# Kernel tuning notes

Hardware: AMD Instinct MI355X
Metric: run time of the kernel (lower is better)

The kernel has to match this reference:

```python
import jax, jax.numpy as jnp
import numpy as np

HIDDEN = 2048
N_HEADS = 32
N_KV = 8
HEAD_DIM = 64
ROPE_THETA = 10000.0


def setup_inputs() -> dict:
    key = jax.random.key(0)
    k0, k1, k2, k3, k4 = jax.random.split(key, 5)
    B, S = 2, 2048
    scale_in = 1.0 / np.sqrt(HIDDEN)
    return {
        "hidden_states": jax.random.normal(k0, (B, S, HIDDEN), dtype=jnp.float32),
        # weights stored [in, out] (transpose of torch Linear.weight)
        "Wq": jax.random.normal(k1, (HIDDEN, N_HEADS * HEAD_DIM), dtype=jnp.float32) * scale_in,
        "Wk": jax.random.normal(k2, (HIDDEN, N_KV * HEAD_DIM), dtype=jnp.float32) * scale_in,
        "Wv": jax.random.normal(k3, (HIDDEN, N_KV * HEAD_DIM), dtype=jnp.float32) * scale_in,
        "Wo": jax.random.normal(k4, (N_HEADS * HEAD_DIM, HIDDEN), dtype=jnp.float32) * scale_in,
    }


def _rope_tables(seq_len, dim, theta):
    inv_freq = 1.0 / (theta ** (jnp.arange(0, dim, 2, dtype=jnp.float32) / dim))
    t = jnp.arange(seq_len, dtype=jnp.float32)
    freqs = jnp.outer(t, inv_freq)              # [S, D/2]
    emb = jnp.concatenate([freqs, freqs], -1)   # [S, D]
    return jnp.cos(emb), jnp.sin(emb)


def _rotate_half(x):
    d = x.shape[-1] // 2
    return jnp.concatenate([-x[..., d:], x[..., :d]], axis=-1)


def reference(hidden_states, Wq, Wk, Wv, Wo):
    B, S, _ = hidden_states.shape
    G = N_HEADS // N_KV  # groups per kv head

    q = (hidden_states @ Wq).reshape(B, S, N_HEADS, HEAD_DIM).transpose(0, 2, 1, 3)  # [B,H,S,D]
    k = (hidden_states @ Wk).reshape(B, S, N_KV, HEAD_DIM).transpose(0, 2, 1, 3)     # [B,KV,S,D]
    v = (hidden_states @ Wv).reshape(B, S, N_KV, HEAD_DIM).transpose(0, 2, 1, 3)

    cos, sin = _rope_tables(S, HEAD_DIM, ROPE_THETA)  # [S,D]
    q = q * cos + _rotate_half(q) * sin
    k = k * cos + _rotate_half(k) * sin

    # GQA without materializing repeated KV: fold q heads into [KV, G]
    qg = q.reshape(B, N_KV, G, S, HEAD_DIM)
    scale = HEAD_DIM ** -0.5
    scores = jnp.einsum("bkgsd,bktd->bkgst", qg, k) * scale  # [B,KV,G,S,S]

    causal = jnp.tril(jnp.ones((S, S), dtype=bool))
    scores = jnp.where(causal, scores, jnp.float32(-1e30))
    probs = jax.nn.softmax(scores, axis=-1)

    out = jnp.einsum("bkgst,bktd->bkgsd", probs, v)          # [B,KV,G,S,D]
    out = out.reshape(B, N_HEADS, S, HEAD_DIM).transpose(0, 2, 1, 3).reshape(B, S, N_HEADS * HEAD_DIM)
    return out @ Wo
```

## Files before the change

kernel.cpp:

```cpp
#include <hip/hip_runtime.h>
#include <cstdint>
#include <cstddef>

typedef __attribute__((ext_vector_type(8))) short short8;
typedef __attribute__((ext_vector_type(4))) float f32x4;
typedef __attribute__((ext_vector_type(16))) float f32x16;

#define MFMA16(a, b, c) __builtin_amdgcn_mfma_f32_16x16x32_bf16((a), (b), (c), 0, 0, 0)
#define MFMA32(a, b, c) __builtin_amdgcn_mfma_f32_32x32x16_bf16((a), (b), (c), 0, 0, 0)

union F2U { float f; unsigned int u; };
union U4S8 { uint4 u4; unsigned short s[8]; short8 v; };

__device__ __forceinline__ unsigned short f2bf(float f) {
  F2U x; x.f = f;
  unsigned int r = x.u + 0x7fffu + ((x.u >> 16) & 1u);
  return (unsigned short)(r >> 16);
}
__device__ __forceinline__ float bf2f(unsigned short s) {
  F2U x; x.u = ((unsigned int)s) << 16;
  return x.f;
}
__device__ __forceinline__ float fexp2(float x) {
  float r; asm("v_exp_f32 %0, %1" : "=v"(r) : "v"(x)); return r;
}
__device__ __forceinline__ unsigned int cvtpk(float lo, float hiv) {
  unsigned int r; asm("v_cvt_pk_bf16_f32 %0, %1, %2" : "=v"(r) : "v"(lo), "v"(hiv)); return r;
}

#define HIDDEN 2048
#define NHEADS 32
#define NKV 8
#define HDIM 64
#define SEQ 2048
#define BATCH 2
#define NTOK (BATCH * SEQ)
#define QKVN 3072
#define QSCALE 0.18033688011117309f

__global__ __launch_bounds__(256) void prep_kernel(const float* __restrict__ X,
                                                   const float* __restrict__ Wq,
                                                   const float* __restrict__ Wk,
                                                   const float* __restrict__ Wv,
                                                   const float* __restrict__ Wo,
                                                   unsigned short* __restrict__ Xb,
                                                   unsigned short* __restrict__ Wqkv_t,
                                                   unsigned short* __restrict__ Wot,
                                                   float* __restrict__ ct,
                                                   float* __restrict__ st) {
  __shared__ unsigned short lt[64][72];
  int bid = blockIdx.x;
  const int t = threadIdx.x;

  if (bid < 256) {
    int idx = bid * 256 + t;
    int s = idx >> 5;
    int i = idx & 31;
    float invf = expf(-(float)i * (9.210340371976184f / 32.0f));
    float f = (float)s * invf;
    ct[idx] = cosf(f);
    st[idx] = sinf(f);
    return;
  }
  bid -= 256;
  if (bid < 4096) {
    size_t i = ((size_t)bid * 256 + t) * 8;
    float4 a0 = *(const float4*)(X + i);
    float4 a1 = *(const float4*)(X + i + 4);
    U4S8 p;
    p.s[0] = f2bf(a0.x); p.s[1] = f2bf(a0.y); p.s[2] = f2bf(a0.z); p.s[3] = f2bf(a0.w);
    p.s[4] = f2bf(a1.x); p.s[5] = f2bf(a1.y); p.s[6] = f2bf(a1.z); p.s[7] = f2bf(a1.w);
    *(short8*)(Xb + i) = p.v;
    return;
  }
  bid -= 4096;
  const float* W; unsigned short* Wt; int N, row_off, bx, by;
  if (bid < 1024)      { W = Wq; Wt = Wqkv_t; N = 2048; row_off = 0;    bx = bid & 31; by = bid >> 5; }
  else if (bid < 1280) { bid -= 1024; W = Wk; Wt = Wqkv_t; N = 512; row_off = 2048; bx = bid & 7; by = bid >> 3; }
  else if (bid < 1536) { bid -= 1280; W = Wv; Wt = Wqkv_t; N = 512; row_off = 2560; bx = bid & 7; by = bid >> 3; }
  else                 { bid -= 1536; W = Wo; Wt = Wot;    N = 2048; row_off = 0;   bx = bid & 31; by = bid >> 5; }
  const int k0 = by * 64, n0 = bx * 64;
  #pragma unroll
  for (int p = 0; p < 4; ++p) {
    int kr = p * 16 + (t >> 4);
    int nc = (t & 15) * 4;
    float4 v = *(const float4*)&W[(size_t)(k0 + kr) * N + n0 + nc];
    lt[nc + 0][kr] = f2bf(v.x);
    lt[nc + 1][kr] = f2bf(v.y);
    lt[nc + 2][kr] = f2bf(v.z);
    lt[nc + 3][kr] = f2bf(v.w);
  }
  __syncthreads();
  #pragma unroll
  for (int p = 0; p < 2; ++p) {
    int nr = p * 32 + (t >> 3);
    int kc = (t & 7) * 8;
    *(short8*)&Wt[(size_t)(row_off + n0 + nr) * HIDDEN + k0 + kc] = *(const short8*)&lt[nr][kc];
  }
}

template<int MODE>
__global__ __launch_bounds__(256) void gemm128_kernel(const unsigned short* __restrict__ Ab,
                                                      const unsigned short* __restrict__ Bt,
                                                      void* __restrict__ Cp,
                                                      int M, int N, int K,
                                                      const float* __restrict__ ct,
                                                      const float* __restrict__ st) {
  __shared__ __align__(16) unsigned short lds_a[128][64];
  __shared__ __align__(16) unsigned short lds_b[128][64];

  const int t = threadIdx.x, lane = t & 63, w = t >> 6;
  const int q32 = lane & 31, hi = lane >> 5;

  const int orig = blockIdx.y * gridDim.x + blockIdx.x;
  const int nwg  = (int)(gridDim.x * gridDim.y);
  const int cpx  = nwg >> 3;
  const int swz  = (orig & 7) * cpx + (orig >> 3);
  const int m0 = (swz / (int)gridDim.x) * 128;
  const int n0 = (swz % (int)gridDim.x) * 128;

  const int wr = (w >> 1) * 64, wc = (w & 1) * 64;

  f32x16 acc[2][2] = {};

  for (int k0 = 0; k0 < K; k0 += 64) {
    __syncthreads();
    #pragma unroll
    for (int c = 0; c < 4; ++c) {
      int row = w * 32 + c * 8 + (lane >> 3);
      int cks = (lane & 7) ^ (row & 7);
      __builtin_amdgcn_global_load_lds(
          (const __attribute__((address_space(1))) unsigned int*)(Ab + (size_t)(m0 + row) * K + k0 + cks * 8),
          (__attribute__((address_space(3))) unsigned int*)&lds_a[w * 32 + c * 8][0], 16, 0, 0);
      __builtin_amdgcn_global_load_lds(
          (const __attribute__((address_space(1))) unsigned int*)(Bt + (size_t)(n0 + row) * K + k0 + cks * 8),
          (__attribute__((address_space(3))) unsigned int*)&lds_b[w * 32 + c * 8][0], 16, 0, 0);
    }
    __syncthreads();

    #pragma unroll
    for (int kq = 0; kq < 4; ++kq) {
      short8 af[2], bf[2];
      #pragma unroll
      for (int i = 0; i < 2; ++i) {
        int row = wr + i * 32 + q32;
        af[i] = *(const short8*)((const char*)&lds_a[0][0] + row * 128 + (((kq * 2 + hi) ^ (row & 7)) * 16));
      }
      #pragma unroll
      for (int j = 0; j < 2; ++j) {
        int row = wc + j * 32 + q32;
        bf[j] = *(const short8*)((const char*)&lds_b[0][0] + row * 128 + (((kq * 2 + hi) ^ (row & 7)) * 16));
      }
      acc[0][0] = MFMA32(af[0], bf[0], acc[0][0]);
      acc[0][1] = MFMA32(af[0], bf[1], acc[0][1]);
      acc[1][0] = MFMA32(af[1], bf[0], acc[1][0]);
      acc[1][1] = MFMA32(af[1], bf[1], acc[1][1]);
    }
  }

  if constexpr (MODE == 0) {
    #pragma unroll
    for (int i = 0; i < 2; ++i)
      #pragma unroll
      for (int j = 0; j < 2; ++j)
        #pragma unroll
        for (int r = 0; r < 16; ++r) {
          int row = m0 + wr + i * 32 + (r & 3) + 8 * (r >> 2) + 4 * hi;
          int col = n0 + wc + j * 32 + q32;
          ((float*)Cp)[(size_t)row * N + col] = acc[i][j][r];
        }
  } else {
    const bool isV = (n0 >= 2560);
    const bool isQ = (n0 < 2048);
    #pragma unroll
    for (int i = 0; i < 2; ++i)
      #pragma unroll
      for (int r = 0; r < 16; ++r) {
        int row = m0 + wr + i * 32 + (r & 3) + 8 * (r >> 2) + 4 * hi;
        int s_tok = row & (SEQ - 1);
        float cc = 0.f, ss = 0.f;
        if (!isV) {
          cc = ct[s_tok * 32 + q32];
          ss = st[s_tok * 32 + q32];
        }
        #pragma unroll
        for (int j = 0; j < 2; ++j) {
          int col = n0 + wc + j * 32 + q32;
          float v = acc[i][j][r];
          float o;
          if (isV) {
            o = v;
          } else {
            float pp = acc[i][j ^ 1][r];
            o = (j == 0) ? (v * cc - pp * ss) : (v * cc + pp * ss);
            if (isQ) o *= QSCALE;
          }
          ((unsigned short*)Cp)[(size_t)row * N + col] = f2bf(o);
        }
      }
  }
}

__global__ __launch_bounds__(256) void v_pack_kernel(const unsigned short* __restrict__ QKV,
                                                     unsigned short* __restrict__ Vt) {
  int idx = blockIdx.x * 256 + threadIdx.x;
  int m = idx >> 9;
  int c = idx & 511;
  int b = m >> 11, s = m & 2047;
  int kv = c >> 6, d = c & 63;
  Vt[(((size_t)(b * NKV + kv)) * HDIM + d) * SEQ + s] = QKV[(size_t)m * QKVN + 2560 + c];
}

#define KVBLK 64

__global__ __launch_bounds__(512, 4) void flash_kernel(const unsigned short* __restrict__ QKV,
                                                       const unsigned short* __restrict__ Vt,
                                                       unsigned short* __restrict__ Ob) {
  const int bx = blockIdx.x;
  const int h = blockIdx.y;
  const int b = blockIdx.z;
  const int kv = h >> 2;
  const int t = threadIdx.x;
  const int lane = t & 63;
  const int w = t >> 6;
  const int p = w >> 1;
  const int kh = w & 1;
  const int q = lane & 31;
  const int hi = lane >> 5;

  __shared__ __align__(16) char smem[34816];
  unsigned short* Klds = (unsigned short*)smem;
  unsigned short* Vlds = (unsigned short*)(smem + 16384);
  float* mlArea = (float*)(smem + 32768);

  const unsigned short* Kg = QKV + (size_t)b * SEQ * QKVN + 2048 + kv * 64;
  const unsigned short* Vg = Vt + ((size_t)(b * NKV + kv)) * HDIM * SEQ;
  const unsigned short* Qh = QKV + (size_t)b * SEQ * QKVN + h * 64;

  const int srow = w * 8 + (lane >> 3);
  const int scks = (lane & 7) ^ (srow & 7);
  const unsigned short* Ksrc = Kg + (size_t)srow * QKVN + scks * 8;
  const unsigned short* Vsrc = Vg + (size_t)srow * SEQ + scks * 8;

  #define STAGE_KV(buf, kt0)                                                              \
    do {                                                                                  \
      __builtin_amdgcn_global_load_lds(                                                   \
          (const __attribute__((address_space(1))) unsigned int*)(Ksrc + (size_t)(kt0) * QKVN), \
          (__attribute__((address_space(3))) unsigned int*)(Klds + (buf) * 4096 + w * 512), 16, 0, 0); \
      __builtin_amdgcn_global_load_lds(                                                   \
          (const __attribute__((address_space(1))) unsigned int*)(Vsrc + (kt0)),          \
          (__attribute__((address_space(3))) unsigned int*)(Vlds + (buf) * 4096 + w * 512), 16, 0, 0); \
    } while (0)

  #pragma unroll 1
  for (int seg = 0; seg < 2; ++seg) {
    const int qb = seg ? bx : (15 - bx);
    const int wq0 = qb * 128 + p * 32;

    short8 qf[4];
    #pragma unroll
    for (int f = 0; f < 4; ++f)
      qf[f] = *(const short8*)&Qh[(size_t)(wq0 + q) * QKVN + f * 16 + hi * 8];

    f32x16 o0 = {}, o1 = {};
    float m_run = -1e30f, l_run = 0.f;

    const int nt_blk = qb * 2 + 2;

    __syncthreads();
    STAGE_KV(0, 0);
    __syncthreads();
    int cur = 0;

    for (int tt = 0; tt < nt_blk; ++tt) {
      if (tt + 1 < nt_blk) STAGE_KV(cur ^ 1, (tt + 1) * KVBLK);

      const int kbase = tt * KVBLK + kh * 32;
      if (kbase <= wq0 + 31) {
        const unsigned short* Kt = Klds + cur * 4096;
        const unsigned short* Vl = Vlds + cur * 4096;

        f32x16 s = {};
        __builtin_amdgcn_s_setprio(1);
        #pragma unroll
        for (int f = 0; f < 4; ++f) {
          short8 kf = *(const short8*)(Kt + (kh * 32 + q) * 64 + (((f * 2 + hi) ^ (q & 7)) * 8));
          s = MFMA32(kf, qf[f], s);
        }
        __builtin_amdgcn_s_setprio(0);

        if (kbase + 31 > wq0) {
          #pragma unroll
          for (int r = 0; r < 16; ++r) {
            int kl = (r & 3) + 8 * (r >> 2) + 4 * hi;
            if (kbase + kl > wq0 + q) s[r] = -1e30f;
          }
        }

        float mt = -1e30f;
        #pragma unroll
        for (int r = 0; r < 16; ++r) mt = fmaxf(mt, s[r]);
        mt = fmaxf(mt, __shfl_xor(mt, 32, 64));

        const bool resc = __any(mt > m_run + 11.0f);
        if (resc) {
          float mn = fmaxf(m_run, mt);
          float alpha = fexp2(m_run - mn);
          m_run = mn;
          l_run *= alpha;
          #pragma unroll
          for (int r = 0; r < 16; ++r) { o0[r] *= alpha; o1[r] *= alpha; }
        }
        float ls = 0.f;
        #pragma unroll
        for (int r = 0; r < 16; ++r) {
          float pp = fexp2(s[r] - m_run);
          s[r] = pp;
          ls += pp;
        }
        ls += __shfl_xor(ls, 32, 64);
        l_run += ls;

        unsigned int own[8];
        #pragma unroll
        for (int g = 0; g < 8; ++g)
          own[g] = cvtpk(s[2 * g], s[2 * g + 1]);

        __builtin_amdgcn_s_setprio(1);
        {
          unsigned int pa0 = own[0], pb0 = own[2];
          unsigned int pa1 = own[1], pb1 = own[3];
          asm("v_permlane32_swap_b32 %0, %1" : "+v"(pa0), "+v"(pb0));
          asm("v_permlane32_swap_b32 %0, %1" : "+v"(pa1), "+v"(pb1));
          U4S8 pfv;
          pfv.u4.x = pa0;
          pfv.u4.y = pa1;
          pfv.u4.z = pb0;
          pfv.u4.w = pb1;
          int co = ((kh * 4 + hi) ^ (q & 7)) * 8;
          short8 vf0 = *(const short8*)(Vl + q * 64 + co);
          short8 vf1 = *(const short8*)(Vl + (32 + q) * 64 + co);
          o0 = MFMA32(vf0, pfv.v, o0);
          o1 = MFMA32(vf1, pfv.v, o1);
        }
        {
          unsigned int pa0 = own[4], pb0 = own[6];
          unsigned int pa1 = own[5], pb1 = own[7];
          asm("v_permlane32_swap_b32 %0, %1" : "+v"(pa0), "+v"(pb0));
          asm("v_permlane32_swap_b32 %0, %1" : "+v"(pa1), "+v"(pb1));
          U4S8 pfv;
          pfv.u4.x = pa0;
          pfv.u4.y = pa1;
          pfv.u4.z = pb0;
          pfv.u4.w = pb1;
          int co = ((kh * 4 + 2 + hi) ^ (q & 7)) * 8;
          short8 vf0 = *(const short8*)(Vl + q * 64 + co);
          short8 vf1 = *(const short8*)(Vl + (32 + q) * 64 + co);
          o0 = MFMA32(vf0, pfv.v, o0);
          o1 = MFMA32(vf1, pfv.v, o1);
        }
        __builtin_amdgcn_s_setprio(0);
      }

      __syncthreads();
      cur ^= 1;
    }

    if (hi == 0) {
      mlArea[(w * 32 + q) * 2 + 0] = m_run;
      mlArea[(w * 32 + q) * 2 + 1] = l_run;
    }
    __syncthreads();
    const int wo = p * 2 + (kh ^ 1);
    float m_oth = mlArea[(wo * 32 + q) * 2 + 0];
    float l_oth = mlArea[(wo * 32 + q) * 2 + 1];
    float m_tot = fmaxf(m_run, m_oth);
    float alf = fexp2(m_run - m_tot);
    float l_tot = l_run * alf + l_oth * fexp2(m_oth - m_tot);
    #pragma unroll
    for (int r = 0; r < 16; ++r) { o0[r] *= alf; o1[r] *= alf; }

    float* oArea = (float*)smem + (size_t)p * 2048;
    if (kh == 1) {
      float* dst = oArea + lane * 32;
      #pragma unroll
      for (int r = 0; r < 16; ++r) { dst[r] = o0[r]; dst[16 + r] = o1[r]; }
    }
    __syncthreads();
    if (kh == 0) {
      const float* src = oArea + lane * 32;
      #pragma unroll
      for (int r = 0; r < 16; ++r) { o0[r] += src[r]; o1[r] += src[16 + r]; }
    }
    __syncthreads();

    if (kh == 0) {
      unsigned short* lo = (unsigned short*)smem + (size_t)p * 2304;
      float inv = 1.0f / l_tot;
      #pragma unroll
      for (int gg = 0; gg < 8; ++gg) {
        int r = 2 * gg;
        int dl = (r & 3) + 8 * (r >> 2) + 4 * hi;
        unsigned int w0 = (unsigned int)f2bf(o0[r] * inv) | ((unsigned int)f2bf(o0[r + 1] * inv) << 16);
        unsigned int w1 = (unsigned int)f2bf(o1[r] * inv) | ((unsigned int)f2bf(o1[r + 1] * inv) << 16);
        *(unsigned int*)&lo[q * 72 + dl] = w0;
        *(unsigned int*)&lo[q * 72 + 32 + dl] = w1;
      }
      {
        int row = lane >> 1;
        int ch = (lane & 1) * 32;
        uint4 x0 = *(const uint4*)&lo[row * 72 + ch + 0];
        uint4 x1 = *(const uint4*)&lo[row * 72 + ch + 8];
        uint4 x2 = *(const uint4*)&lo[row * 72 + ch + 16];
        uint4 x3 = *(const uint4*)&lo[row * 72 + ch + 24];
        unsigned short* dst = &Ob[(size_t)(b * SEQ + wq0 + row) * (NHEADS * HDIM) + h * HDIM + ch];
        *(uint4*)(dst + 0)  = x0;
        *(uint4*)(dst + 8)  = x1;
        *(uint4*)(dst + 16) = x2;
        *(uint4*)(dst + 24) = x3;
      }
    }
  }
}

extern "C" void kernel_launch(void* const* d_in, const int* in_sizes, int n_in,
                              void* d_out, int out_size, void* d_ws, size_t ws_size,
                              hipStream_t stream) {
  const float* X  = (const float*)d_in[0];
  const float* Wq = (const float*)d_in[1];
  const float* Wk = (const float*)d_in[2];
  const float* Wv = (const float*)d_in[3];
  const float* Wo = (const float*)d_in[4];
  float* out = (float*)d_out;

  char* ws = (char*)d_ws;
  size_t off = 0;
  auto carve = [&](size_t bytes) -> void* {
    void* p = ws + off;
    off += (bytes + 255) & ~(size_t)255;
    return p;
  };
  float* rope_cos = (float*)carve((size_t)SEQ * 32 * 4);
  float* rope_sin = (float*)carve((size_t)SEQ * 32 * 4);
  unsigned short* Xb     = (unsigned short*)carve((size_t)NTOK * HIDDEN * 2);
  unsigned short* Wqkv_t = (unsigned short*)carve((size_t)QKVN * HIDDEN * 2);
  unsigned short* Wot    = (unsigned short*)carve((size_t)HIDDEN * HIDDEN * 2);
  unsigned short* QKVb   = (unsigned short*)carve((size_t)NTOK * QKVN * 2);
  unsigned short* Vt     = (unsigned short*)carve((size_t)BATCH * NKV * HDIM * SEQ * 2);
  unsigned short* Ob     = Xb;

  prep_kernel<<<dim3(6912), dim3(256), 0, stream>>>(
      X, Wq, Wk, Wv, Wo, Xb, Wqkv_t, Wot, rope_cos, rope_sin);

  gemm128_kernel<1><<<dim3(QKVN / 128, NTOK / 128), dim3(256), 0, stream>>>(
      Xb, Wqkv_t, QKVb, NTOK, QKVN, HIDDEN, rope_cos, rope_sin);

  v_pack_kernel<<<dim3((NTOK * NKV * HDIM) / 256), dim3(256), 0, stream>>>(QKVb, Vt);

  flash_kernel<<<dim3(8, NHEADS, BATCH), dim3(512), 0, stream>>>(QKVb, Vt, Ob);

  gemm128_kernel<0><<<dim3(HIDDEN / 128, NTOK / 128), dim3(256), 0, stream>>>(
      Ob, Wot, out, NTOK, HIDDEN, HIDDEN, nullptr, nullptr);
}
```

Before: 203.5 us.

## Use 256x256 double-buffered direct-to-LDS GEMM for QKV and tile V transpose

Replaces the QKV projection GEMM with a new 256x256-tile, 512-thread kernel. It double-buffers K slices in 128KB of LDS via global_load_lds and brackets MFMA bursts with barriers and setprio, while keeping the fused RoPE/scale epilogue. This aims to raise data reuse and overlap loads with compute. The V pack kernel is also rewritten to transpose through an LDS tile with vectorized reads and writes instead of scattered 2-byte stores. The QKV grid shrinks to 12x16 blocks and the 128KB of LDS allows only one block per CU, so occupancy and wave balance across CUs may suffer.

```diff
diff --git a/kernel.cpp b/kernel.cpp
--- a/kernel.cpp
+++ b/kernel.cpp
@@ -99,13 +99,138 @@
   }
 }
 
-template<int MODE>
+__global__ __launch_bounds__(512, 2) void gemm256_kernel(const unsigned short* __restrict__ Ab,
+                                                         const unsigned short* __restrict__ Bt,
+                                                         unsigned short* __restrict__ Cp,
+                                                         const float* __restrict__ ct,
+                                                         const float* __restrict__ st) {
+  __shared__ __align__(16) char smem[131072];
+
+  const int t = threadIdx.x, lane = t & 63, w = t >> 6;
+  const int q32 = lane & 31, hi = lane >> 5;
+  const int K = HIDDEN, N = QKVN;
+
+  const int orig = blockIdx.y * gridDim.x + blockIdx.x;
+  const int nwg  = (int)(gridDim.x * gridDim.y);
+  const int cpx  = nwg >> 3;
+  const int swz  = (orig & 7) * cpx + (orig >> 3);
+  const int m0 = (swz / (int)gridDim.x) * 256;
+  const int n0 = (swz % (int)gridDim.x) * 256;
+
+  const int wr = (w >> 2) * 128;
+  const int wc = (w & 3) * 64;
+
+  const int srow0 = w * 8 + (lane >> 3);
+  const int scks  = (lane & 7) ^ (srow0 & 7);
+  const unsigned short* PA = Ab + (size_t)(m0 + srow0) * K + scks * 8;
+  const unsigned short* PB = Bt + (size_t)(n0 + srow0) * K + scks * 8;
+
+  #define STAGE256(buf, k0)                                                                \
+    do {                                                                                   \
+      _Pragma("unroll")                                                                    \
+      for (int c = 0; c < 4; ++c) {                                                        \
+        __builtin_amdgcn_global_load_lds(                                                  \
+            (const __attribute__((address_space(1))) unsigned int*)(PA + (size_t)c * 64 * K + (k0)), \
+            (__attribute__((address_space(3))) unsigned int*)(smem + (buf) * 32768 + (c * 64 + w * 8) * 128), 16, 0, 0); \
+        __builtin_amdgcn_global_load_lds(                                                  \
+            (const __attribute__((address_space(1))) unsigned int*)(PB + (size_t)c * 64 * K + (k0)), \
+            (__attribute__((address_space(3))) unsigned int*)(smem + 65536 + (buf) * 32768 + (c * 64 + w * 8) * 128), 16, 0, 0); \
+      }                                                                                    \
+    } while (0)
+
+  f32x16 acc[4][2] = {};
+  short8 bfr[2][4];
+
+  const int NT = K / 64;
+
+  STAGE256(0, 0);
+  asm volatile("s_waitcnt vmcnt(0)");
+  __builtin_amdgcn_s_barrier();
+
+  for (int tt = 0; tt < NT; ++tt) {
+    const int buf = tt & 1;
+    const char* LA = smem + buf * 32768;
+    const char* LB = smem + 65536 + buf * 32768;
+
+    if (tt + 1 < NT) STAGE256(buf ^ 1, (tt + 1) * 64);
+    #pragma unroll
+    for (int j = 0; j < 2; ++j) {
+      int row = wc + j * 32 + q32;
+      #pragma unroll
+      for (int kq = 0; kq < 4; ++kq)
+        bfr[j][kq] = *(const short8*)(LB + row * 128 + (((kq * 2 + hi) ^ (row & 7)) * 16));
+    }
+    {
+      short8 af[4];
+      int row = wr + q32;
+      #pragma unroll
+      for (int kq = 0; kq < 4; ++kq)
+        af[kq] = *(const short8*)(LA + row * 128 + (((kq * 2 + hi) ^ (row & 7)) * 16));
+      __builtin_amdgcn_s_barrier();
+      __builtin_amdgcn_s_setprio(1);
+      #pragma unroll
+      for (int kq = 0; kq < 4; ++kq) {
+        acc[0][0] = MFMA32(af[kq], bfr[0][kq], acc[0][0]);
+        acc[0][1] = MFMA32(af[kq], bfr[1][kq], acc[0][1]);
+      }
+      __builtin_amdgcn_s_setprio(0);
+      __builtin_amdgcn_s_barrier();
+    }
+    #pragma unroll
+    for (int i = 1; i < 4; ++i) {
+      short8 af[4];
+      int row = wr + i * 32 + q32;
+      #pragma unroll
+      for (int kq = 0; kq < 4; ++kq)
+        af[kq] = *(const short8*)(LA + row * 128 + (((kq * 2 + hi) ^ (row & 7)) * 16));
+      __builtin_amdgcn_s_barrier();
+      __builtin_amdgcn_s_setprio(1);
+      #pragma unroll
+      for (int kq = 0; kq < 4; ++kq) {
+        acc[i][0] = MFMA32(af[kq], bfr[0][kq], acc[i][0]);
+        acc[i][1] = MFMA32(af[kq], bfr[1][kq], acc[i][1]);
+      }
+      __builtin_amdgcn_s_setprio(0);
+      __builtin_amdgcn_s_barrier();
+    }
+    asm volatile("s_waitcnt vmcnt(0)");
+    __builtin_amdgcn_s_barrier();
+  }
+
+  const bool isV = (n0 >= 2560);
+  const bool isQ = (n0 + 255 < 2048);
+  #pragma unroll
+  for (int i = 0; i < 4; ++i)
+    #pragma unroll
+    for (int r = 0; r < 16; ++r) {
+      int row = m0 + wr + i * 32 + (r & 3) + 8 * (r >> 2) + 4 * hi;
+      int s_tok = row & (SEQ - 1);
+      float cc = 0.f, ss = 0.f;
+      if (!isV) {
+        cc = ct[s_tok * 32 + q32];
+        ss = st[s_tok * 32 + q32];
+      }
+      #pragma unroll
+      for (int j = 0; j < 2; ++j) {
+        int col = n0 + wc + j * 32 + q32;
+        float v = acc[i][j][r];
+        float o;
+        if (isV) {
+          o = v;
+        } else {
+          float pp = acc[i][j ^ 1][r];
+          o = (j == 0) ? (v * cc - pp * ss) : (v * cc + pp * ss);
+          if (isQ) o *= QSCALE;
+        }
+        Cp[(size_t)row * N + col] = f2bf(o);
+      }
+    }
+}
+
 __global__ __launch_bounds__(256) void gemm128_kernel(const unsigned short* __restrict__ Ab,
                                                       const unsigned short* __restrict__ Bt,
-                                                      void* __restrict__ Cp,
-                                                      int M, int N, int K,
-                                                      const float* __restrict__ ct,
-                                                      const float* __restrict__ st) {
+                                                      float* __restrict__ Cp,
+                                                      int M, int N, int K) {
   __shared__ __align__(16) unsigned short lds_a[128][64];
   __shared__ __align__(16) unsigned short lds_b[128][64];
 
@@ -158,57 +283,43 @@
     }
   }
 
-  if constexpr (MODE == 0) {
-    #pragma unroll
-    for (int i = 0; i < 2; ++i)
-      #pragma unroll
-      for (int j = 0; j < 2; ++j)
-        #pragma unroll
-        for (int r = 0; r < 16; ++r) {
-          int row = m0 + wr + i * 32 + (r & 3) + 8 * (r >> 2) + 4 * hi;
-          int col = n0 + wc + j * 32 + q32;
-          ((float*)Cp)[(size_t)row * N + col] = acc[i][j][r];
-        }
-  } else {
-    const bool isV = (n0 >= 2560);
-    const bool isQ = (n0 < 2048);
-    #pragma unroll
-    for (int i = 0; i < 2; ++i)
+  #pragma unroll
+  for (int i = 0; i < 2; ++i)
+    #pragma unroll
+    for (int j = 0; j < 2; ++j)
       #pragma unroll
       for (int r = 0; r < 16; ++r) {
         int row = m0 + wr + i * 32 + (r & 3) + 8 * (r >> 2) + 4 * hi;
-        int s_tok = row & (SEQ - 1);
-        float cc = 0.f, ss = 0.f;
-        if (!isV) {
-          cc = ct[s_tok * 32 + q32];
-          ss = st[s_tok * 32 + q32];
-        }
-        #pragma unroll
-        for (int j = 0; j < 2; ++j) {
-          int col = n0 + wc + j * 32 + q32;
-          float v = acc[i][j][r];
-          float o;
-          if (isV) {
-            o = v;
-          } else {
-            float pp = acc[i][j ^ 1][r];
-            o = (j == 0) ? (v * cc - pp * ss) : (v * cc + pp * ss);
-            if (isQ) o *= QSCALE;
-          }
-          ((unsigned short*)Cp)[(size_t)row * N + col] = f2bf(o);
-        }
-      }
-  }
+        int col = n0 + wc + j * 32 + q32;
+        Cp[(size_t)row * N + col] = acc[i][j][r];
+      }
 }
 
 __global__ __launch_bounds__(256) void v_pack_kernel(const unsigned short* __restrict__ QKV,
                                                      unsigned short* __restrict__ Vt) {
-  int idx = blockIdx.x * 256 + threadIdx.x;
-  int m = idx >> 9;
-  int c = idx & 511;
-  int b = m >> 11, s = m & 2047;
-  int kv = c >> 6, d = c & 63;
-  Vt[(((size_t)(b * NKV + kv)) * HDIM + d) * SEQ + s] = QKV[(size_t)m * QKVN + 2560 + c];
+  __shared__ unsigned short lt[64][72];
+  const int t = threadIdx.x;
+  const int s0 = blockIdx.x * 64;
+  const int kv = blockIdx.y;
+  const int b = blockIdx.z;
+
+  #pragma unroll
+  for (int pass = 0; pass < 2; ++pass) {
+    int tok = pass * 32 + (t >> 3);
+    int d = (t & 7) * 8;
+    short8 v = *(const short8*)&QKV[(size_t)(b * SEQ + s0 + tok) * QKVN + 2560 + kv * 64 + d];
+    U4S8 u; u.v = v;
+    #pragma unroll
+    for (int e = 0; e < 8; ++e) lt[d + e][tok] = u.s[e];
+  }
+  __syncthreads();
+  {
+    int d = t >> 2;
+    int scol = (t & 3) * 16;
+    unsigned short* dst = &Vt[(((size_t)(b * NKV + kv)) * HDIM + d) * SEQ + s0 + scol];
+    *(uint4*)(dst + 0) = *(const uint4*)&lt[d][scol + 0];
+    *(uint4*)(dst + 8) = *(const uint4*)&lt[d][scol + 8];
+  }
 }
 
 #define KVBLK 64
@@ -452,13 +563,13 @@
   prep_kernel<<<dim3(6912), dim3(256), 0, stream>>>(
       X, Wq, Wk, Wv, Wo, Xb, Wqkv_t, Wot, rope_cos, rope_sin);
 
-  gemm128_kernel<1><<<dim3(QKVN / 128, NTOK / 128), dim3(256), 0, stream>>>(
-      Xb, Wqkv_t, QKVb, NTOK, QKVN, HIDDEN, rope_cos, rope_sin);
-
-  v_pack_kernel<<<dim3((NTOK * NKV * HDIM) / 256), dim3(256), 0, stream>>>(QKVb, Vt);
+  gemm256_kernel<<<dim3(QKVN / 256, NTOK / 256), dim3(512), 0, stream>>>(
+      Xb, Wqkv_t, QKVb, rope_cos, rope_sin);
+
+  v_pack_kernel<<<dim3(SEQ / 64, NKV, BATCH), dim3(256), 0, stream>>>(QKVb, Vt);
 
   flash_kernel<<<dim3(8, NHEADS, BATCH), dim3(512), 0, stream>>>(QKVb, Vt, Ob);
 
-  gemm128_kernel<0><<<dim3(HIDDEN / 128, NTOK / 128), dim3(256), 0, stream>>>(
-      Ob, Wot, out, NTOK, HIDDEN, HIDDEN, nullptr, nullptr);
-}
+  gemm128_kernel<<<dim3(HIDDEN / 128, NTOK / 128), dim3(256), 0, stream>>>(
+      Ob, Wot, out, NTOK, HIDDEN, HIDDEN);
+}
```

Measured after the change: 204.5 us. About the same (+0.5%).
